# Optimization experiments

Measured on AMD Instinct MI355X. Metric: run time of the kernel, lower is better.

## Reference

```python
import jax, jax.numpy as jnp
import numpy as np

V = 6890   # SMPL vertices
J = 24     # SMPL joints
NB = 10    # betas
P = 207    # pose blendshape basis = (J-1)*9
B = 1024
PARENTS = np.array([-1, 0, 0, 0, 1, 2, 3, 4, 5, 6, 7, 8, 9, 9, 9, 12, 13, 14, 16, 17, 18, 19, 20, 21])


def setup_inputs() -> dict:
    key = jax.random.key(0)
    ks = jax.random.split(key, 9)
    pose_axis_angle = jax.random.normal(ks[0], (B, 69), dtype=jnp.float32) * 0.2
    betas = jax.random.normal(ks[1], (B, NB), dtype=jnp.float32)
    global_orient = jax.random.normal(ks[2], (B, 3), dtype=jnp.float32) * 0.2
    v_template = jax.random.normal(ks[3], (V, 3), dtype=jnp.float32)
    shapedirs = jax.random.normal(ks[4], (V, 3, NB), dtype=jnp.float32) * 0.01
    posedirs = jax.random.normal(ks[5], (P, V * 3), dtype=jnp.float32) * 0.01
    jr = jax.random.uniform(ks[6], (J, V), dtype=jnp.float32)
    J_regressor = jr / jr.sum(-1, keepdims=True)
    jr17 = jax.random.uniform(ks[7], (17, V), dtype=jnp.float32)
    J_regressor_h36m = jr17 / jr17.sum(-1, keepdims=True)
    w = jax.random.uniform(ks[8], (V, J), dtype=jnp.float32)
    lbs_weights = w / w.sum(-1, keepdims=True)
    return {
        'pose_axis_angle': pose_axis_angle, 'betas': betas, 'global_orient': global_orient,
        'v_template': v_template, 'shapedirs': shapedirs, 'posedirs': posedirs,
        'J_regressor': J_regressor, 'J_regressor_h36m': J_regressor_h36m,
        'lbs_weights': lbs_weights,
    }


def rodrigues(rvec):
    # rvec: [N,3] axis-angle -> [N,3,3] rotation matrices
    angle = jnp.linalg.norm(rvec + 1e-8, axis=-1, keepdims=True)  # [N,1]
    axis = rvec / angle
    s = jnp.sin(angle)[..., None]
    c = jnp.cos(angle)[..., None]
    rx, ry, rz = axis[..., 0], axis[..., 1], axis[..., 2]
    z = jnp.zeros_like(rx)
    K = jnp.stack([z, -rz, ry, rz, z, -rx, -ry, rx, z], axis=-1).reshape(-1, 3, 3)
    I = jnp.eye(3, dtype=rvec.dtype)
    return I + s * K + (1.0 - c) * (K @ K)


def _lbs(pose_axis_angle, betas, global_orient, v_template, shapedirs, posedirs,
         J_regressor, J_regressor_h36m, lbs_weights):
    b = betas.shape[0]
    full_pose = jnp.concatenate([global_orient, pose_axis_angle], axis=1)  # [B,72]
    # shape blendshapes
    v_shaped = v_template + jnp.einsum('bl,vkl->bvk', betas, shapedirs)    # [B,V,3]
    Jrest = jnp.einsum('jv,bvk->bjk', J_regressor, v_shaped)               # [B,J,3]
    # pose to rotation matrices
    rot_mats = rodrigues(full_pose.reshape(-1, 3)).reshape(b, J, 3, 3)
    I3 = jnp.eye(3, dtype=rot_mats.dtype)
    pose_feature = (rot_mats[:, 1:] - I3).reshape(b, P)                    # [B,207]
    v_posed = v_shaped + (pose_feature @ posedirs).reshape(b, V, 3)
    # kinematic tree FK
    rel = Jrest.at[:, 1:].add(-Jrest[:, PARENTS[1:]])                      # relative joint offsets
    T = (jnp.zeros((b, J, 4, 4), dtype=rot_mats.dtype)
         .at[..., :3, :3].set(rot_mats)
         .at[..., :3, 3].set(rel)
         .at[..., 3, 3].set(1.0))
    chain = [T[:, 0]]
    for i in range(1, J):
        chain.append(chain[int(PARENTS[i])] @ T[:, i])
    G = jnp.stack(chain, axis=1)                                           # [B,J,4,4]
    posed_joints = G[:, :, :3, 3]
    # remove rest-pose joint locations to get skinning transforms
    A = G.at[:, :, :3, 3].add(-jnp.einsum('bjmn,bjn->bjm', G[:, :, :3, :3], Jrest))
    # linear blend skinning
    Tv = jnp.einsum('vj,bjmn->bvmn', lbs_weights, A)                       # [B,V,4,4]
    verts = jnp.einsum('bvmn,bvn->bvm', Tv[:, :, :3, :3], v_posed) + Tv[:, :, :3, 3]
    joints_from_verts = jnp.einsum('jv,bvk->bjk', J_regressor_h36m, verts)
    return verts, posed_joints, rot_mats, joints_from_verts


def reference(pose_axis_angle, betas, global_orient, v_template, shapedirs, posedirs,
              J_regressor, J_regressor_h36m, lbs_weights):
    verts, joints, rot_mats, jfv = _lbs(pose_axis_angle, betas, global_orient, v_template,
                                        shapedirs, posedirs, J_regressor, J_regressor_h36m,
                                        lbs_weights)
    # transl is None -> root-center (root is detached in torch)
    root = jax.lax.stop_gradient(joints[:, :1])
    root17 = jax.lax.stop_gradient(jfv[:, :1])
    return verts - root, joints - root, rot_mats, jfv - root17
```

## Files before the change

kernel.cpp:

```cpp
#include <hip/hip_runtime.h>
#include <hip/hip_bf16.h>

constexpr int kB  = 1024;
constexpr int kV  = 6890;
constexpr int kJ  = 24;
constexpr int kNB = 10;
constexpr int kP  = 207;
constexpr int kH  = 17;

constexpr int kN   = kV * 3;
constexpr int kKP  = 224;
constexpr int kNT  = 1296;
constexpr int kNP  = kNT * 16;
constexpr int kVC  = 862;

constexpr int kJsBlocks = kJ * 8;
constexpr int kPbBlocks = kNP / 64;
constexpr int kJB  = 4;
constexpr int kLbsTB = 8;

constexpr size_t O_VERTS  = 0;
constexpr size_t O_JOINTS = (size_t)kB * kV * 3;
constexpr size_t O_ROT    = O_JOINTS + (size_t)kB * kJ * 3;
constexpr size_t O_JFV    = O_ROT + (size_t)kB * kJ * 9;

constexpr size_t WS_JSP  = 0;
constexpr size_t WS_ROOT = 8192;
constexpr size_t WS_ABHI = 16384;
constexpr size_t WS_ABLO = WS_ABHI + 262144;
constexpr size_t WS_ASWZ = WS_ABLO + 262144;
constexpr size_t WS_BSWZ = WS_ASWZ + 114688;

typedef __attribute__((ext_vector_type(8))) short short8;
typedef __attribute__((ext_vector_type(4))) float float4v;

__device__ __forceinline__ unsigned short f2bf(float f) {
    unsigned u = __float_as_uint(f);
    unsigned r = (u + 0x7FFFu + ((u >> 16) & 1u)) >> 16;
    return (unsigned short)r;
}
__device__ __forceinline__ float bf2f(unsigned short h) {
    return __uint_as_float((unsigned)h << 16);
}

__device__ __forceinline__ bool amb0_is_weights(const float* __restrict__ amb0) {
    float s = 0.f;
    #pragma unroll
    for (int i = 0; i < kJ; i++) s += amb0[i];
    return fabsf(s - 1.0f) < 0.5f;
}

__device__ __forceinline__ size_t a_idx(int mtile, int minr, int k) {
    int kt = k >> 5, quad = (k >> 3) & 3, kin = k & 7;
    return ((size_t)(mtile * 7 + kt)) * 512 + (size_t)(quad * 128 + minr * 8 + kin);
}

__global__ __launch_bounds__(256) void k_sfb(
    const float* __restrict__ amb0,
    const float* __restrict__ amb1,
    const float* __restrict__ sd,
    const float* __restrict__ vt,
    const float* __restrict__ pd,
    float* __restrict__ partial,
    unsigned short* __restrict__ bswz)
{
    __shared__ unsigned short lds[kKP][68];
    __shared__ float red[4][33];

    int t = threadIdx.x;

    if (blockIdx.x < kJsBlocks) {
        const float* Jreg = amb0_is_weights(amb0) ? amb1 : amb0;
        int j = blockIdx.x >> 3;
        int c = blockIdx.x & 7;
        int lane = t & 63;
        int wave = t >> 6;

        float acc[33];
        #pragma unroll
        for (int i = 0; i < 33; i++) acc[i] = 0.f;

        int vend = min(kVC * (c + 1), kV);
        for (int v = kVC * c + t; v < vend; v += 256) {
            float w = Jreg[j * kV + v];
            const float* sdp = sd + (size_t)v * 30;
            #pragma unroll
            for (int k = 0; k < 3; k++) {
                #pragma unroll
                for (int l = 0; l < kNB; l++)
                    acc[k * 11 + l] += w * sdp[k * 10 + l];
                acc[k * 11 + 10] += w * vt[v * 3 + k];
            }
        }
        #pragma unroll
        for (int off = 32; off > 0; off >>= 1) {
            #pragma unroll
            for (int i = 0; i < 33; i++)
                acc[i] += __shfl_down(acc[i], off, 64);
        }
        if (lane == 0) {
            #pragma unroll
            for (int i = 0; i < 33; i++) red[wave][i] = acc[i];
        }
        __syncthreads();
        if (t < 33) {
            float s = red[0][t] + red[1][t] + red[2][t] + red[3][t];
            partial[((size_t)j * 8 + c) * 33 + t] = s;
        }
    } else {
        int g = blockIdx.x - kJsBlocks;
        int n0 = g * 64;

        for (int kbase = 0; kbase < kKP; kbase += 4) {
            int k = kbase + (t >> 6);
            int nl = t & 63;
            int n = n0 + nl;
            float val = 0.f;
            if (n < kN) {
                if (k < kP)                 val = pd[(size_t)k * kN + n];
                else if (k < kP + kNB)      val = sd[(size_t)n * kNB + (k - kP)];
                else if (k == kP + kNB)     val = vt[n];
            }
            lds[k][nl] = f2bf(val);
        }
        __syncthreads();

        #pragma unroll 1
        for (int tt = 0; tt < 4; tt++) {
            int ntile = g * 4 + tt;
            #pragma unroll 1
            for (int kt = 0; kt < 7; kt++) {
                size_t base = ((size_t)ntile * 7 + kt) * 512;
                #pragma unroll
                for (int u = 0; u < 2; u++) {
                    int e = t * 2 + u;
                    int quad = e >> 7, rem = e & 127;
                    int nin = rem >> 3, kin = rem & 7;
                    int k = kt * 32 + quad * 8 + kin;
                    bswz[base + e] = lds[k][tt * 16 + nin];
                }
            }
        }
    }
}

__global__ __launch_bounds__(64) void k_pose(
    const float* __restrict__ pose,
    const float* __restrict__ betas,
    const float* __restrict__ gor,
    const float* __restrict__ jsp,
    float* __restrict__ wsRoot,
    unsigned short* __restrict__ aswz,
    unsigned short* __restrict__ abhi,
    unsigned short* __restrict__ ablo,
    float* __restrict__ out)
{
    __shared__ float Rsh[kJ][9];
    __shared__ float Jr[kJ][3];
    __shared__ float G[kJ][12];
    __shared__ float Ash[kJ][12];

    int b = blockIdx.x;
    int t = threadIdx.x;
    int mtile = b >> 4, minr = b & 15;

    if (t < kJ) {
        float rx, ry, rz;
        if (t == 0) {
            rx = gor[b * 3 + 0]; ry = gor[b * 3 + 1]; rz = gor[b * 3 + 2];
        } else {
            int o = b * 69 + (t - 1) * 3;
            rx = pose[o]; ry = pose[o + 1]; rz = pose[o + 2];
        }
        float ex = rx + 1e-8f, ey = ry + 1e-8f, ez = rz + 1e-8f;
        float ang = sqrtf(ex * ex + ey * ey + ez * ez);
        float x = rx / ang, y = ry / ang, z = rz / ang;
        float s = sinf(ang), c = cosf(ang), oc = 1.0f - c;
        float r[9];
        r[0] = 1.0f - oc * (y * y + z * z);
        r[1] = -s * z + oc * (x * y);
        r[2] =  s * y + oc * (x * z);
        r[3] =  s * z + oc * (x * y);
        r[4] = 1.0f - oc * (x * x + z * z);
        r[5] = -s * x + oc * (y * z);
        r[6] = -s * y + oc * (x * z);
        r[7] =  s * x + oc * (y * z);
        r[8] = 1.0f - oc * (x * x + y * y);
        #pragma unroll
        for (int i = 0; i < 9; i++) Rsh[t][i] = r[i];
        float* ro = out + O_ROT + (size_t)b * (kJ * 9) + (size_t)t * 9;
        #pragma unroll
        for (int i = 0; i < 9; i++) ro[i] = r[i];
        if (t >= 1) {
            #pragma unroll
            for (int i = 0; i < 9; i++) {
                int k = (t - 1) * 9 + i;
                float val = r[i] - ((i == 0 || i == 4 || i == 8) ? 1.0f : 0.0f);
                aswz[a_idx(mtile, minr, k)] = f2bf(val);
            }
        }
        float bt[kNB];
        #pragma unroll
        for (int l = 0; l < kNB; l++) bt[l] = betas[b * kNB + l];
        #pragma unroll
        for (int k2 = 0; k2 < 3; k2++) {
            float row[11];
            #pragma unroll
            for (int i = 0; i < 11; i++) row[i] = 0.f;
            #pragma unroll
            for (int c8 = 0; c8 < 8; c8++) {
                const float* pp = jsp + ((size_t)t * 8 + c8) * 33 + k2 * 11;
                #pragma unroll
                for (int i = 0; i < 11; i++) row[i] += pp[i];
            }
            float acc = row[10];
            #pragma unroll
            for (int l = 0; l < kNB; l++) acc += bt[l] * row[l];
            Jr[t][k2] = acc;
        }
    } else if (t < 41 + kJ) {
        int idx = t - kJ;
        if (idx < 17) {
            int k = kP + idx;
            float val = 0.f;
            if (idx < kNB)          val = betas[b * kNB + idx];
            else if (k == kP + kNB) val = 1.0f;
            aswz[a_idx(mtile, minr, k)] = f2bf(val);
        }
    }
    __syncthreads();

    if (t == 0) {
        const int par[kJ] = {-1,0,0,0,1,2,3,4,5,6,7,8,9,9,9,12,13,14,16,17,18,19,20,21};
        #pragma unroll
        for (int m = 0; m < 3; m++) {
            #pragma unroll
            for (int n = 0; n < 3; n++) G[0][m * 4 + n] = Rsh[0][m * 3 + n];
            G[0][m * 4 + 3] = Jr[0][m];
        }
        for (int i = 1; i < kJ; i++) {
            int p = par[i];
            float rel[3];
            #pragma unroll
            for (int k = 0; k < 3; k++) rel[k] = Jr[i][k] - Jr[p][k];
            #pragma unroll
            for (int m = 0; m < 3; m++) {
                float g0 = G[p][m * 4 + 0], g1 = G[p][m * 4 + 1], g2 = G[p][m * 4 + 2];
                #pragma unroll
                for (int n = 0; n < 3; n++) {
                    G[i][m * 4 + n] = g0 * Rsh[i][0 * 3 + n]
                                    + g1 * Rsh[i][1 * 3 + n]
                                    + g2 * Rsh[i][2 * 3 + n];
                }
                G[i][m * 4 + 3] = g0 * rel[0] + g1 * rel[1] + g2 * rel[2]
                                + G[p][m * 4 + 3];
            }
        }
    }
    __syncthreads();

    if (t < kJ) {
        float* jo = out + O_JOINTS + (size_t)b * (kJ * 3) + (size_t)t * 3;
        #pragma unroll
        for (int m = 0; m < 3; m++) {
            float g0 = G[t][m * 4 + 0], g1 = G[t][m * 4 + 1], g2 = G[t][m * 4 + 2];
            float tr = G[t][m * 4 + 3]
                     - (g0 * Jr[t][0] + g1 * Jr[t][1] + g2 * Jr[t][2]);
            Ash[t][m * 4 + 0] = g0;
            Ash[t][m * 4 + 1] = g1;
            Ash[t][m * 4 + 2] = g2;
            Ash[t][m * 4 + 3] = tr;
            jo[m] = G[t][m * 4 + 3] - G[0][m * 4 + 3];
        }
        if (t == 0) {
            #pragma unroll
            for (int k = 0; k < 3; k++) wsRoot[b * 3 + k] = G[0][k * 4 + 3];
        }
    }
    __syncthreads();

    {
        short8 h8, l8;
        #pragma unroll
        for (int e = 0; e < 8; e++) {
            int j = (t >> 4) * 8 + e;
            int m = t & 15;
            float val = (j < kJ && m < 12) ? Ash[j][m] : 0.f;
            unsigned short h = f2bf(val);
            h8[e] = (short)h;
            l8[e] = (short)f2bf(val - bf2f(h));
        }
        *(short8*)(abhi + (size_t)b * 512 + t * 8) = h8;
        *(short8*)(ablo + (size_t)b * 512 + t * 8) = l8;
    }
}

__global__ __launch_bounds__(256) void k_gemm(
    const unsigned short* __restrict__ A,
    const unsigned short* __restrict__ B,
    float* __restrict__ out)
{
    int tid = threadIdx.x;
    int lane = tid & 63;
    int wid = tid >> 6;
    int m0t = blockIdx.y * 8 + (wid >> 1) * 4;
    int n0t = blockIdx.x * 8 + (wid & 1) * 4;

    float4v acc[4][4];
    #pragma unroll
    for (int i = 0; i < 4; i++)
        #pragma unroll
        for (int j = 0; j < 4; j++)
            acc[i][j] = (float4v){0.f, 0.f, 0.f, 0.f};

    #pragma unroll
    for (int kt = 0; kt < 7; kt++) {
        short8 a[4], b[4];
        #pragma unroll
        for (int i = 0; i < 4; i++)
            a[i] = *(const short8*)(A + ((size_t)(m0t + i) * 7 + kt) * 512 + lane * 8);
        #pragma unroll
        for (int j = 0; j < 4; j++)
            b[j] = *(const short8*)(B + ((size_t)(n0t + j) * 7 + kt) * 512 + lane * 8);
        #pragma unroll
        for (int i = 0; i < 4; i++)
            #pragma unroll
            for (int j = 0; j < 4; j++)
                acc[i][j] = __builtin_amdgcn_mfma_f32_16x16x32_bf16(
                    a[i], b[j], acc[i][j], 0, 0, 0);
    }

    int rbase = (lane >> 4) * 4;
    int col = lane & 15;
    #pragma unroll
    for (int i = 0; i < 4; i++) {
        #pragma unroll
        for (int j = 0; j < 4; j++) {
            int n = (n0t + j) * 16 + col;
            if (n < kN) {
                #pragma unroll
                for (int reg = 0; reg < 4; reg++) {
                    int brow = (m0t + i) * 16 + rbase + reg;
                    out[O_VERTS + (size_t)brow * kN + n] = acc[i][j][reg];
                }
            }
        }
    }
}

__global__ __launch_bounds__(256) void k_lbs(
    const float* __restrict__ amb0,
    const float* __restrict__ amb1,
    const unsigned short* __restrict__ abhi,
    const unsigned short* __restrict__ ablo,
    const float* __restrict__ wsRoot,
    float* __restrict__ out)
{
    const float* W = amb0_is_weights(amb0) ? amb0 : amb1;
    __shared__ float ldsT[256 * 13];

    int t = threadIdx.x;
    int lane = t & 63, w = t >> 6;
    int vb = blockIdx.x;
    int b0 = blockIdx.y * kLbsTB;
    int chunk = lane >> 4;

    short8 wh[4], wl[4];
    #pragma unroll
    for (int i = 0; i < 4; i++) {
        int row = vb * 256 + (w * 4 + i) * 16 + (lane & 15);
        float vals[8];
        if (chunk < 3 && row < kV) {
            const float4v* p = (const float4v*)(W + (size_t)row * kJ + chunk * 8);
            float4v x0 = p[0], x1 = p[1];
            vals[0] = x0[0]; vals[1] = x0[1]; vals[2] = x0[2]; vals[3] = x0[3];
            vals[4] = x1[0]; vals[5] = x1[1]; vals[6] = x1[2]; vals[7] = x1[3];
        } else {
            #pragma unroll
            for (int e = 0; e < 8; e++) vals[e] = 0.f;
        }
        #pragma unroll
        for (int e = 0; e < 8; e++) {
            unsigned short h = f2bf(vals[e]);
            wh[i][e] = (short)h;
            wl[i][e] = (short)f2bf(vals[e] - bf2f(h));
        }
    }

    int v = vb * 256 + t;
    bool act = (v < kV);
    int crow = (lane >> 4) * 4;
    int ccol = lane & 15;

    #pragma unroll 1
    for (int tb = 0; tb < kLbsTB; tb++) {
        int b = b0 + tb;
        short8 ah = *(const short8*)(abhi + (size_t)b * 512 + lane * 8);
        short8 al = *(const short8*)(ablo + (size_t)b * 512 + lane * 8);

        #pragma unroll
        for (int i = 0; i < 4; i++) {
            float4v acc = (float4v){0.f, 0.f, 0.f, 0.f};
            acc = __builtin_amdgcn_mfma_f32_16x16x32_bf16(wl[i], ah, acc, 0, 0, 0);
            acc = __builtin_amdgcn_mfma_f32_16x16x32_bf16(wh[i], al, acc, 0, 0, 0);
            acc = __builtin_amdgcn_mfma_f32_16x16x32_bf16(wh[i], ah, acc, 0, 0, 0);
            if (ccol < 12) {
                int base = (w * 4 + i) * 16 * 13;
                #pragma unroll
                for (int reg = 0; reg < 4; reg++)
                    ldsT[base + (crow + reg) * 13 + ccol] = acc[reg];
            }
        }
        __syncthreads();

        {
            const float* T = &ldsT[t * 13];
            float r0 = wsRoot[(size_t)b * 3 + 0];
            float r1 = wsRoot[(size_t)b * 3 + 1];
            float r2 = wsRoot[(size_t)b * 3 + 2];
            if (act) {
                float* op = out + O_VERTS + ((size_t)b * kV + v) * 3;
                float x = op[0], y = op[1], z = op[2];
                float o0 = T[0] * x + T[1] * y + T[2]  * z + T[3]  - r0;
                float o1 = T[4] * x + T[5] * y + T[6]  * z + T[7]  - r1;
                float o2 = T[8] * x + T[9] * y + T[10] * z + T[11] - r2;
                op[0] = o0; op[1] = o1; op[2] = o2;
            }
        }
        __syncthreads();
    }
}

__global__ __launch_bounds__(1024) void k_jfv(
    const float* __restrict__ Jh,
    const float* __restrict__ verts,
    float* __restrict__ out)
{
    int b0 = blockIdx.x * kJB;
    int t = threadIdx.x;
    int wave = t >> 6, lane = t & 63;
    int j0 = wave;
    bool has2 = (wave == 0);

    float acc0[kJB][3], acc1[kJB][3];
    #pragma unroll
    for (int bb = 0; bb < kJB; bb++)
        #pragma unroll
        for (int k = 0; k < 3; k++) { acc0[bb][k] = 0.f; acc1[bb][k] = 0.f; }

    const float* Jr0 = Jh + (size_t)j0 * kV;
    const float* Jr1 = Jh + (size_t)16 * kV;

    for (int v = lane; v < kV; v += 64) {
        float w0 = Jr0[v];
        float w1 = has2 ? Jr1[v] : 0.f;
        #pragma unroll
        for (int bb = 0; bb < kJB; bb++) {
            const float* vp = verts + ((size_t)(b0 + bb) * kV + v) * 3;
            float vx = vp[0], vy = vp[1], vz = vp[2];
            acc0[bb][0] += w0 * vx; acc0[bb][1] += w0 * vy; acc0[bb][2] += w0 * vz;
            acc1[bb][0] += w1 * vx; acc1[bb][1] += w1 * vy; acc1[bb][2] += w1 * vz;
        }
    }
    #pragma unroll
    for (int off = 32; off > 0; off >>= 1) {
        #pragma unroll
        for (int bb = 0; bb < kJB; bb++)
            #pragma unroll
            for (int k = 0; k < 3; k++) {
                acc0[bb][k] += __shfl_down(acc0[bb][k], off, 64);
                acc1[bb][k] += __shfl_down(acc1[bb][k], off, 64);
            }
    }
    __shared__ float fin[kJB][52];
    if (lane == 0) {
        #pragma unroll
        for (int bb = 0; bb < kJB; bb++)
            #pragma unroll
            for (int k = 0; k < 3; k++) {
                fin[bb][j0 * 3 + k] = acc0[bb][k];
                if (has2) fin[bb][48 + k] = acc1[bb][k];
            }
    }
    __syncthreads();
    if (t < kJB * 51) {
        int bb = t / 51, i = t - bb * 51;
        out[O_JFV + (size_t)(b0 + bb) * 51 + i] = fin[bb][i] - fin[bb][i % 3];
    }
}

extern "C" void kernel_launch(void* const* d_in, const int* in_sizes, int n_in,
                              void* d_out, int out_size, void* d_ws, size_t ws_size,
                              hipStream_t stream) {
    const float *pose = nullptr, *betas = nullptr, *gor = nullptr, *vt = nullptr,
                *sd = nullptr, *pd = nullptr, *Jh = nullptr;
    const float *amb0 = nullptr, *amb1 = nullptr;
    for (int i = 0; i < n_in; i++) {
        const float* p = (const float*)d_in[i];
        switch (in_sizes[i]) {
            case 70656:   pose  = p; break;
            case 10240:   betas = p; break;
            case 3072:    gor   = p; break;
            case 20670:   vt    = p; break;
            case 206700:  sd    = p; break;
            case 4278690: pd    = p; break;
            case 117130:  Jh    = p; break;
            case 165360:  if (!amb0) amb0 = p; else amb1 = p; break;
            default: break;
        }
    }

    float* ws = (float*)d_ws;
    float* jsp     = ws + WS_JSP;
    float* wsRoot  = ws + WS_ROOT;
    unsigned short* abhi = (unsigned short*)(ws + WS_ABHI);
    unsigned short* ablo = (unsigned short*)(ws + WS_ABLO);
    unsigned short* aswz = (unsigned short*)(ws + WS_ASWZ);
    unsigned short* bswz = (unsigned short*)(ws + WS_BSWZ);

    float* out = (float*)d_out;

    k_sfb  <<<dim3(kJsBlocks + kPbBlocks), dim3(256), 0, stream>>>(
        amb0, amb1, sd, vt, pd, jsp, bswz);
    k_pose <<<dim3(kB),                 dim3(64),  0, stream>>>(
        pose, betas, gor, jsp, wsRoot, aswz, abhi, ablo, out);
    k_gemm <<<dim3(kNT / 8, kB / 128),  dim3(256), 0, stream>>>(aswz, bswz, out);
    k_lbs  <<<dim3(27, kB / kLbsTB),    dim3(256), 0, stream>>>(
        amb0, amb1, abhi, ablo, wsRoot, out);
    k_jfv  <<<dim3(kB / kJB),           dim3(1024), 0, stream>>>(
        Jh, out + O_VERTS, out);
}
```

Measured before the change: 283.7 us.

## Restructure J_regressor_h36m reduction with LDS-staged weight chunks and per-wave batch split

Rewrites the k_jfv kernel so each wave handles one batch element and a subset of the 17 joints. J_regressor_h36m rows are staged in double-buffered shared-memory chunks, so each vertex coordinate is loaded once per wave instead of once per joint-wave. This cuts redundant global reads of the vertex array, which were repeated 16 times per block. In exchange it adds a per-chunk barrier and LDS traffic, and the prefetch into the other buffer is plain synchronous loads.

```diff
diff --git a/kernel.cpp b/kernel.cpp
--- a/kernel.cpp
+++ b/kernel.cpp
@@ -18,6 +18,7 @@
 constexpr int kPbBlocks = kNP / 64;
 constexpr int kJB  = 4;
 constexpr int kLbsTB = 8;
+constexpr int kCH  = 384;
 
 constexpr size_t O_VERTS  = 0;
 constexpr size_t O_JOINTS = (size_t)kB * kV * 3;
@@ -436,56 +437,89 @@
     const float* __restrict__ verts,
     float* __restrict__ out)
 {
+    __shared__ float jsh[2][kH][kCH];
+    __shared__ float fin[kJB][52];
+
     int b0 = blockIdx.x * kJB;
     int t = threadIdx.x;
     int wave = t >> 6, lane = t & 63;
-    int j0 = wave;
-    bool has2 = (wave == 0);
-
-    float acc0[kJB][3], acc1[kJB][3];
-    #pragma unroll
-    for (int bb = 0; bb < kJB; bb++)
-        #pragma unroll
-        for (int k = 0; k < 3; k++) { acc0[bb][k] = 0.f; acc1[bb][k] = 0.f; }
-
-    const float* Jr0 = Jh + (size_t)j0 * kV;
-    const float* Jr1 = Jh + (size_t)16 * kV;
-
-    for (int v = lane; v < kV; v += 64) {
-        float w0 = Jr0[v];
-        float w1 = has2 ? Jr1[v] : 0.f;
-        #pragma unroll
-        for (int bb = 0; bb < kJB; bb++) {
-            const float* vp = verts + ((size_t)(b0 + bb) * kV + v) * 3;
+    int bb = wave & 3;
+    int g  = wave >> 2;
+    bool has5 = (g == 0);
+
+    const float* vbase = verts + (size_t)(b0 + bb) * kV * 3;
+
+    float acc[5][3];
+    #pragma unroll
+    for (int rr = 0; rr < 5; rr++)
+        #pragma unroll
+        for (int k = 0; k < 3; k++) acc[rr][k] = 0.f;
+
+    constexpr int nc = (kV + kCH - 1) / kCH;
+
+    for (int e = t; e < kH * kCH; e += 1024) {
+        int r = e / kCH, i = e - r * kCH;
+        jsh[0][r][i] = (i < kV) ? Jh[(size_t)r * kV + i] : 0.f;
+    }
+    __syncthreads();
+
+    #pragma unroll 1
+    for (int c = 0; c < nc; c++) {
+        int cur = c & 1;
+        if (c + 1 < nc) {
+            int v0n = (c + 1) * kCH;
+            for (int e = t; e < kH * kCH; e += 1024) {
+                int r = e / kCH, i = e - r * kCH;
+                int v = v0n + i;
+                jsh[cur ^ 1][r][i] = (v < kV) ? Jh[(size_t)r * kV + v] : 0.f;
+            }
+        }
+        int v0 = c * kCH;
+        int chlen = min(kCH, kV - v0);
+        for (int vi = lane; vi < chlen; vi += 64) {
+            const float* vp = vbase + (size_t)(v0 + vi) * 3;
             float vx = vp[0], vy = vp[1], vz = vp[2];
-            acc0[bb][0] += w0 * vx; acc0[bb][1] += w0 * vy; acc0[bb][2] += w0 * vz;
-            acc1[bb][0] += w1 * vx; acc1[bb][1] += w1 * vy; acc1[bb][2] += w1 * vz;
-        }
-    }
+            #pragma unroll
+            for (int rr = 0; rr < 4; rr++) {
+                float wj = jsh[cur][g + rr * 4][vi];
+                acc[rr][0] += wj * vx;
+                acc[rr][1] += wj * vy;
+                acc[rr][2] += wj * vz;
+            }
+            if (has5) {
+                float wj = jsh[cur][16][vi];
+                acc[4][0] += wj * vx;
+                acc[4][1] += wj * vy;
+                acc[4][2] += wj * vz;
+            }
+        }
+        __syncthreads();
+    }
+
     #pragma unroll
     for (int off = 32; off > 0; off >>= 1) {
         #pragma unroll
-        for (int bb = 0; bb < kJB; bb++)
-            #pragma unroll
-            for (int k = 0; k < 3; k++) {
-                acc0[bb][k] += __shfl_down(acc0[bb][k], off, 64);
-                acc1[bb][k] += __shfl_down(acc1[bb][k], off, 64);
-            }
-    }
-    __shared__ float fin[kJB][52];
+        for (int rr = 0; rr < 5; rr++)
+            #pragma unroll
+            for (int k = 0; k < 3; k++)
+                acc[rr][k] += __shfl_down(acc[rr][k], off, 64);
+    }
     if (lane == 0) {
         #pragma unroll
-        for (int bb = 0; bb < kJB; bb++)
-            #pragma unroll
-            for (int k = 0; k < 3; k++) {
-                fin[bb][j0 * 3 + k] = acc0[bb][k];
-                if (has2) fin[bb][48 + k] = acc1[bb][k];
-            }
+        for (int rr = 0; rr < 4; rr++)
+            #pragma unroll
+            for (int k = 0; k < 3; k++)
+                fin[bb][(g + rr * 4) * 3 + k] = acc[rr][k];
+        if (has5) {
+            #pragma unroll
+            for (int k = 0; k < 3; k++)
+                fin[bb][48 + k] = acc[4][k];
+        }
     }
     __syncthreads();
     if (t < kJB * 51) {
-        int bb = t / 51, i = t - bb * 51;
-        out[O_JFV + (size_t)(b0 + bb) * 51 + i] = fin[bb][i] - fin[bb][i % 3];
+        int b2 = t / 51, i = t - b2 * 51;
+        out[O_JFV + (size_t)(b0 + b2) * 51 + i] = fin[b2][i] - fin[b2][i % 3];
     }
 }
 
```

Result: slower. 302.5 us (+6.6%).

## Repartition jfv kernel so each wave handles all 17 joints over a vertex slice

Applied to the files above, without the earlier changes.

The joints-from-verts kernel now gives each wave one batch element and a quarter of the vertices, and each wave accumulates all 17 regressor rows. Before, each wave owned one joint row and re-read the vertices of all four batches. Each vertex is now loaded once per batch instead of once per joint per wave, which cuts redundant global reads of verts. In exchange it holds 51 accumulators per thread, does more shuffle reductions and adds a cross-wave partial sum in shared memory, so register pressure rises.

```diff
diff --git a/kernel.cpp b/kernel.cpp
--- a/kernel.cpp
+++ b/kernel.cpp
@@ -18,6 +18,7 @@
 constexpr int kPbBlocks = kNP / 64;
 constexpr int kJB  = 4;
 constexpr int kLbsTB = 8;
+constexpr int kSL  = 1723;
 
 constexpr size_t O_VERTS  = 0;
 constexpr size_t O_JOINTS = (size_t)kB * kV * 3;
@@ -436,56 +437,59 @@
     const float* __restrict__ verts,
     float* __restrict__ out)
 {
+    __shared__ float part[16][kH * 3];
+
     int b0 = blockIdx.x * kJB;
     int t = threadIdx.x;
     int wave = t >> 6, lane = t & 63;
-    int j0 = wave;
-    bool has2 = (wave == 0);
-
-    float acc0[kJB][3], acc1[kJB][3];
-    #pragma unroll
-    for (int bb = 0; bb < kJB; bb++)
-        #pragma unroll
-        for (int k = 0; k < 3; k++) { acc0[bb][k] = 0.f; acc1[bb][k] = 0.f; }
-
-    const float* Jr0 = Jh + (size_t)j0 * kV;
-    const float* Jr1 = Jh + (size_t)16 * kV;
-
-    for (int v = lane; v < kV; v += 64) {
-        float w0 = Jr0[v];
-        float w1 = has2 ? Jr1[v] : 0.f;
-        #pragma unroll
-        for (int bb = 0; bb < kJB; bb++) {
-            const float* vp = verts + ((size_t)(b0 + bb) * kV + v) * 3;
-            float vx = vp[0], vy = vp[1], vz = vp[2];
-            acc0[bb][0] += w0 * vx; acc0[bb][1] += w0 * vy; acc0[bb][2] += w0 * vz;
-            acc1[bb][0] += w1 * vx; acc1[bb][1] += w1 * vy; acc1[bb][2] += w1 * vz;
-        }
-    }
+    int bb = wave >> 2;
+    int sl = wave & 3;
+
+    const float* vbase = verts + (size_t)(b0 + bb) * kV * 3;
+
+    float acc[kH][3];
+    #pragma unroll
+    for (int r = 0; r < kH; r++)
+        #pragma unroll
+        for (int k = 0; k < 3; k++) acc[r][k] = 0.f;
+
+    int vend = min(kSL * (sl + 1), kV);
+    for (int v = kSL * sl + lane; v < vend; v += 64) {
+        const float* vp = vbase + (size_t)v * 3;
+        float vx = vp[0], vy = vp[1], vz = vp[2];
+        #pragma unroll
+        for (int r = 0; r < kH; r++) {
+            float wj = Jh[(size_t)r * kV + v];
+            acc[r][0] += wj * vx;
+            acc[r][1] += wj * vy;
+            acc[r][2] += wj * vz;
+        }
+    }
+
     #pragma unroll
     for (int off = 32; off > 0; off >>= 1) {
         #pragma unroll
-        for (int bb = 0; bb < kJB; bb++)
-            #pragma unroll
-            for (int k = 0; k < 3; k++) {
-                acc0[bb][k] += __shfl_down(acc0[bb][k], off, 64);
-                acc1[bb][k] += __shfl_down(acc1[bb][k], off, 64);
-            }
-    }
-    __shared__ float fin[kJB][52];
+        for (int r = 0; r < kH; r++)
+            #pragma unroll
+            for (int k = 0; k < 3; k++)
+                acc[r][k] += __shfl_down(acc[r][k], off, 64);
+    }
     if (lane == 0) {
         #pragma unroll
-        for (int bb = 0; bb < kJB; bb++)
-            #pragma unroll
-            for (int k = 0; k < 3; k++) {
-                fin[bb][j0 * 3 + k] = acc0[bb][k];
-                if (has2) fin[bb][48 + k] = acc1[bb][k];
-            }
+        for (int r = 0; r < kH; r++)
+            #pragma unroll
+            for (int k = 0; k < 3; k++)
+                part[wave][r * 3 + k] = acc[r][k];
     }
     __syncthreads();
-    if (t < kJB * 51) {
-        int bb = t / 51, i = t - bb * 51;
-        out[O_JFV + (size_t)(b0 + bb) * 51 + i] = fin[bb][i] - fin[bb][i % 3];
+    if (t < kJB * (kH * 3)) {
+        int b2 = t / (kH * 3), i = t - b2 * (kH * 3);
+        float s  = part[b2 * 4 + 0][i] + part[b2 * 4 + 1][i]
+                 + part[b2 * 4 + 2][i] + part[b2 * 4 + 3][i];
+        int k = i % 3;
+        float sk = part[b2 * 4 + 0][k] + part[b2 * 4 + 1][k]
+                 + part[b2 * 4 + 2][k] + part[b2 * 4 + 3][k];
+        out[O_JFV + (size_t)(b0 + b2) * 51 + i] = s - sk;
     }
 }
 
```

New measurement: 258.6 us. 8.9% less time.
